# Kernel optimization log

Measured on AMD Instinct MI355X. Metric: run time of the kernel, lower is better.

Reference implementation:

```python
import jax, jax.numpy as jnp
import numpy as np

B, L, IN, H, E = 64, 255, 32, 256, 128
PAD = (L - 1) // 2
DN = ('NCH', 'OIH', 'NCH')


def setup_inputs() -> dict:
    ks = jax.random.split(jax.random.key(0), 10)
    r = lambda k, shp, s=0.05: jax.random.normal(k, shp, dtype=jnp.float32) * s
    return {
        's': jax.random.normal(ks[0], (B, L, IN), dtype=jnp.float32),
        'conv1_w': r(ks[1], (H, IN, L)),
        'conv1_b': r(ks[2], (H,)),
        'bn_gamma': jnp.ones((H,), jnp.float32),
        'bn_beta': jnp.zeros((H,), jnp.float32),
        'conv2_w': r(ks[3], (E, H, L)),
        'conv2_b': r(ks[4], (E,)),
        'pw1': r(ks[5], (E, H, L)),   # stacked Linear(L, H) weights, one per channel
        'pb1': r(ks[6], (E, H)),
        'pw2': r(ks[7], (E, 2, H)),   # stacked Linear(H, 2) weights
        'pb2': r(ks[8], (E, 2)),
    }


def reference(s, conv1_w, conv1_b, bn_gamma, bn_beta, conv2_w, conv2_b, pw1, pb1, pw2, pb2):
    x = jnp.transpose(s, (0, 2, 1))  # (B, IN, T)
    h = jax.lax.conv_general_dilated(x, conv1_w, (1,), [(PAD, PAD)], dimension_numbers=DN)
    h = jax.nn.relu(h + conv1_b[None, :, None])
    # BatchNorm1d in training mode: biased batch stats over (N, T)
    mean = h.mean(axis=(0, 2), keepdims=True)
    var = ((h - mean) ** 2).mean(axis=(0, 2), keepdims=True)
    h = (h - mean) * jax.lax.rsqrt(var + 1e-5) * bn_gamma[None, :, None] + bn_beta[None, :, None]
    z = jax.lax.conv_general_dilated(h, conv2_w, (1,), [(PAD, PAD)], dimension_numbers=DN)
    z = jnp.transpose(z + conv2_b[None, :, None], (0, 2, 1))  # (B, T, E)

    rf = jnp.fft.rfft(z, axis=1)                 # (B, F, E), F = L//2 + 1 == E
    power = jnp.abs(rf)[:, :, 1:] ** 2           # faithful channel-axis slice -> (B, F, E-1)
    freq_bins = jnp.fft.rfftfreq(L)[1:]          # (F-1,) == (E-1,)
    frequency = jnp.sum(freq_bins * power, axis=1) / jnp.sum(power, axis=1)  # (B, E-1)
    amplitude = 2.0 * jnp.sqrt(jnp.sum(power, axis=1)) / L                    # (B, E-1)
    offset = rf.real[:, :, 0] / L                                              # (B, E)

    # batched per-channel 2-layer MLP (replaces Python loop over embedding_dim)
    hmid = jax.nn.relu(jnp.einsum('btc,cht->bch', z, pw1) + pb1[None])  # (B, E, H)
    ang = jnp.einsum('bch,coh->bco', hmid, pw2) + pb2[None]             # (B, E, 2)
    phase = jnp.arctan2(ang[:, :, 1], ang[:, :, 0])                     # (B, E)
    return (amplitude, phase, frequency, offset)
```

## Files before the change

### kernel.cpp

```cpp
#include <hip/hip_runtime.h>
#include <math.h>

#define TB   64
#define TT   255
#define TIN  32
#define NH   256
#define NE   128
#define NK   255
#define NPAD 127

#define NF    384
#define NBINS 193
#define NFC   386
#define FCP   416
#define HCH   64

typedef __attribute__((ext_vector_type(8))) short short8;
typedef __attribute__((ext_vector_type(4))) float float4v;

#define WSB_WP1  0u
#define WSB_Z    0u
#define WSB_HF   8388608u
#define WSB_HMID 8388608u
#define WSB_W2S  25165824u
#define WSB_HSP  37814272u
#define WSB_ZSP  44138496u
#define WSB_BD   56786944u
#define WSB_BW   57182208u
#define WSB_BIT  57577472u
#define WSB_BN   58003456u

#define O_AMP   0u
#define O_PHASE 8128u
#define O_FREQ  16320u
#define O_OFF   24448u

static __device__ __forceinline__ unsigned short f2bf(float f) {
  unsigned int u = __float_as_uint(f);
  unsigned int r = (u + 0x7FFFu + ((u >> 16) & 1u)) >> 16;
  return (unsigned short)r;
}
static __device__ __forceinline__ float bf2f(unsigned short s) {
  return __uint_as_float(((unsigned int)s) << 16);
}
static __device__ __forceinline__ short8 as_s8(uint4 v) {
  union { uint4 u; short8 s; } c; c.u = v; return c.s;
}

static __device__ __forceinline__ void split3(float x, unsigned short& h,
                                              unsigned short& l, unsigned short& m2) {
  h = f2bf(x);
  float r1 = x - bf2f(h);
  l = f2bf(r1);
  m2 = f2bf(r1 - bf2f(l));
}

static __device__ __forceinline__ void stage8(unsigned int* __restrict__ U, int r,
                                              int p0, const float* __restrict__ v) {
  const int sw = r & 7;
  const int base = r * 32;
#pragma unroll
  for (int q = 0; q < 4; ++q) {
    float x0 = v[2 * q], x1 = v[2 * q + 1];
    unsigned short h0 = f2bf(x0), h1 = f2bf(x1);
    unsigned short l0 = f2bf(x0 - bf2f(h0)), l1 = f2bf(x1 - bf2f(h1));
    int p = p0 + q;
    U[base + ((((p >> 2) ^ sw) << 2) | (p & 3))] = (unsigned int)h0 | ((unsigned int)h1 << 16);
    U[base + (((((p >> 2) + 4) ^ sw) << 2) | (p & 3))] = (unsigned int)l0 | ((unsigned int)l1 << 16);
  }
}

static __device__ __forceinline__ void stage8_3(unsigned int* __restrict__ U,
                                                unsigned int* __restrict__ U2, int r,
                                                int p0, const float* __restrict__ v) {
  const int sw = r & 7;
  const int base = r * 32;
#pragma unroll
  for (int q = 0; q < 4; ++q) {
    unsigned short h0, l0, m0_, h1, l1, m1_;
    split3(v[2 * q], h0, l0, m0_);
    split3(v[2 * q + 1], h1, l1, m1_);
    int p = p0 + q;
    int shi = (((p >> 2) ^ sw) << 2) | (p & 3);
    int slo = ((((p >> 2) + 4) ^ sw) << 2) | (p & 3);
    U[base + shi] = (unsigned int)h0 | ((unsigned int)h1 << 16);
    U[base + slo] = (unsigned int)l0 | ((unsigned int)l1 << 16);
    U2[base + shi] = (unsigned int)m0_ | ((unsigned int)m1_ << 16);
  }
}
static __device__ __forceinline__ void stage2_3(unsigned int* __restrict__ U,
                                                unsigned int* __restrict__ U2, int r,
                                                int p, float x0, float x1) {
  const int sw = r & 7;
  unsigned short h0, l0, m0_, h1, l1, m1_;
  split3(x0, h0, l0, m0_);
  split3(x1, h1, l1, m1_);
  int shi = (((p >> 2) ^ sw) << 2) | (p & 3);
  int slo = ((((p >> 2) + 4) ^ sw) << 2) | (p & 3);
  U[r * 32 + shi] = (unsigned int)h0 | ((unsigned int)h1 << 16);
  U[r * 32 + slo] = (unsigned int)l0 | ((unsigned int)l1 << 16);
  U2[r * 32 + shi] = (unsigned int)m0_ | ((unsigned int)m1_ << 16);
}
static __device__ __forceinline__ short8 frag(const unsigned short* __restrict__ lds,
                                              int row, int quad, int part) {
  return *(const short8*)&lds[row * 64 + (((quad ^ (part << 2)) ^ (row & 7)) << 3)];
}
#define MF(a, b, c) __builtin_amdgcn_mfma_f32_16x16x32_bf16((a), (b), (c), 0, 0, 0)
#define MF6(accv, ahv, alv, a2v, bhv, blv, b2v) do {                              \
    accv = MF(ahv, bhv, accv);                                                    \
    accv = MF(ahv, blv, accv);                                                    \
    accv = MF(alv, bhv, accv);                                                    \
    accv = MF(alv, blv, accv);                                                    \
    accv = MF(ahv, b2v, accv);                                                    \
    accv = MF(a2v, bhv, accv);                                                    \
  } while (0)

__global__ __launch_bounds__(256) void bn_zero_k(float* __restrict__ bn) {
  bn[threadIdx.x] = 0.f;
  bn[256 + threadIdx.x] = 0.f;
}

__global__ __launch_bounds__(256) void basis_init_k(float* __restrict__ bd,
                                                    float* __restrict__ bw,
                                                    float* __restrict__ bi_t) {
  const int m = blockIdx.x;
  const int t = threadIdx.x;
  const int f = m >> 1, im = m & 1;
  const float C = 6.28318530717958647692f / 384.f;
  int r1 = (f * t) % 384;
  float th1 = C * (float)r1;
  float s1 = sinf(th1), c1 = cosf(th1);
  float vd = im ? -s1 : c1;
  bd[m * 256 + t] = (t == 255) ? 0.f : vd;
  float wgt = (f == 0 || f == 192) ? 1.f : 2.f;
  bi_t[t * FCP + m] = (im ? -s1 * wgt : c1 * wgt) * (1.f / 384.f);
  if (m < FCP - NFC) bi_t[t * FCP + NFC + m] = 0.f;
  int a = f * (t - 127);
  int r2 = a % 384; if (r2 < 0) r2 += 384;
  float th2 = C * (float)r2;
  float vw = im ? sinf(th2) : cosf(th2);
  bw[m * 256 + t] = (t == 255) ? 0.f : vw;
}

__global__ __launch_bounds__(256) void pack1_k(const float* __restrict__ w1,
                                               unsigned int* __restrict__ wp1u) {
  __shared__ float tile[512][33];
  const int et = blockIdx.x, kc = blockIdx.y;
  const int kk0 = kc * 32, cnt = min(32, NK - kk0);
  const int tid = threadIdx.x;
  for (int idx = tid; idx < 512 * 32; idx += 256) {
    int row = idx >> 5, kl = idx & 31;
    if (kl < cnt) {
      int e_l = row >> 5, i_l = row & 31;
      tile[row][kl] = w1[(size_t)((et * 16 + e_l) * TIN + i_l) * NK + kk0 + kl];
    }
  }
  __syncthreads();
  const int lane = tid >> 2, jp = (tid & 3) * 2;
  const int row0 = (lane & 15) * 32 + (lane >> 4) * 8 + jp;
  for (int kl = 0; kl < cnt; ++kl) {
    float w0 = tile[row0][kl], w1v = tile[row0 + 1][kl];
    unsigned short h0 = f2bf(w0), h1 = f2bf(w1v);
    unsigned short l0 = f2bf(w0 - bf2f(h0)), l1 = f2bf(w1v - bf2f(h1));
    size_t base = (size_t)(kk0 + kl) * 8192 + et * 512 + tid;
    wp1u[base] = (unsigned int)h0 | ((unsigned int)h1 << 16);
    wp1u[base + 256] = (unsigned int)l0 | ((unsigned int)l1 << 16);
  }
}

#define C1_ROWS 384
__global__ __launch_bounds__(256, 2) void conv1_mfma(
    const float* __restrict__ s, const unsigned int* __restrict__ wp1u,
    const float* __restrict__ b1v, float* __restrict__ hf, float* __restrict__ bn) {
  __shared__ __align__(16) unsigned short Alds[C1_ROWS * 64];
  const int th = blockIdx.x & 1, chg = blockIdx.x >> 1, b = blockIdx.y;
  const int tid = threadIdx.x, lane = tid & 63, wv = tid >> 6;
  const int quad = lane >> 4, l15 = lane & 15;
  const int tg = wv & 1, eg = wv >> 1;
  unsigned int* Au = (unsigned int*)Alds;

  for (int idx = tid; idx < C1_ROWS * 16; idx += 256) {
    int r = idx >> 4, p = idx & 15;
    int t = th * 128 + r - NPAD;
    float v0 = 0.f, v1 = 0.f;
    if (t >= 0 && t < TT) {
      const float* sp = &s[(size_t)(b * TT + t) * TIN + p * 2];
      v0 = sp[0]; v1 = sp[1];
    }
    unsigned short h0 = f2bf(v0), h1 = f2bf(v1);
    unsigned short l0 = f2bf(v0 - bf2f(h0)), l1 = f2bf(v1 - bf2f(h1));
    int sw = r & 7;
    Au[r * 32 + ((((p >> 2) ^ sw) << 2) | (p & 3))] = (unsigned int)h0 | ((unsigned int)h1 << 16);
    Au[r * 32 + (((((p >> 2) + 4) ^ sw) << 2) | (p & 3))] = (unsigned int)l0 | ((unsigned int)l1 << 16);
  }

#define LOADB1(buf, KK) do {                                                      \
    const uint4* _b = (const uint4*)(wp1u + (size_t)(KK) * 8192u) +               \
                      (chg * 4 + eg * 2) * 128;                                   \
    buf[0] = _b[lane];          buf[1] = _b[64 + lane];                           \
    buf[2] = _b[128 + lane];    buf[3] = _b[192 + lane];                          \
  } while (0)

#define MSTEP1(KK, buf) do {                                                      \
    short8 bh0 = as_s8(buf[0]), bl0 = as_s8(buf[1]);                              \
    short8 bh1 = as_s8(buf[2]), bl1 = as_s8(buf[3]);                              \
    _Pragma("unroll")                                                             \
    for (int mi = 0; mi < 4; ++mi) {                                              \
      const int row = tg * 64 + mi * 16 + l15 + (KK);                             \
      const int sw = row & 7;                                                     \
      short8 ah = *(const short8*)&Alds[row * 64 + ((quad ^ sw) << 3)];           \
      short8 al = *(const short8*)&Alds[row * 64 + (((quad ^ 4) ^ sw) << 3)];     \
      acc[mi][0] = MF(ah, bh0, acc[mi][0]);                                       \
      acc[mi][0] = MF(ah, bl0, acc[mi][0]);                                       \
      acc[mi][0] = MF(al, bh0, acc[mi][0]);                                       \
      acc[mi][1] = MF(ah, bh1, acc[mi][1]);                                       \
      acc[mi][1] = MF(ah, bl1, acc[mi][1]);                                       \
      acc[mi][1] = MF(al, bh1, acc[mi][1]);                                       \
    }                                                                             \
  } while (0)

  uint4 b0[4], b1x[4], b2x[4];
  LOADB1(b0, 0);
  LOADB1(b1x, 1);
  LOADB1(b2x, 2);
  __syncthreads();

  float4v acc[4][2];
#pragma unroll
  for (int mi = 0; mi < 4; ++mi)
#pragma unroll
    for (int ni = 0; ni < 2; ++ni) acc[mi][ni] = (float4v)(0.f);

  for (int kp = 0; kp < 84; ++kp) {
    const int kk = kp * 3;
    MSTEP1(kk, b0);     LOADB1(b0, kk + 3);
    MSTEP1(kk + 1, b1x); LOADB1(b1x, kk + 4);
    MSTEP1(kk + 2, b2x); LOADB1(b2x, kk + 5);
  }
  MSTEP1(252, b0);
  MSTEP1(253, b1x);
  MSTEP1(254, b2x);

  float s1[2] = {0.f, 0.f}, s2[2] = {0.f, 0.f};
#pragma unroll
  for (int mi = 0; mi < 4; ++mi) {
#pragma unroll
    for (int ni = 0; ni < 2; ++ni) {
      int ch = chg * 64 + (eg * 2 + ni) * 16 + l15;
      float bias = b1v[ch];
#pragma unroll
      for (int r = 0; r < 4; ++r) {
        int t = th * 128 + tg * 64 + mi * 16 + quad * 4 + r;
        if (t < TT) {
          float v = fmaxf(acc[mi][ni][r] + bias, 0.f);
          hf[(size_t)(b * 256 + t) * NH + ch] = v;
          s1[ni] += v; s2[ni] += v * v;
        }
      }
    }
  }
#pragma unroll
  for (int ni = 0; ni < 2; ++ni) {
    s1[ni] += __shfl_xor(s1[ni], 16);
    s1[ni] += __shfl_xor(s1[ni], 32);
    s2[ni] += __shfl_xor(s2[ni], 16);
    s2[ni] += __shfl_xor(s2[ni], 32);
    if (quad == 0) {
      int ch = chg * 64 + (eg * 2 + ni) * 16 + l15;
      atomicAdd(&bn[ch], s1[ni]);
      atomicAdd(&bn[256 + ch], s2[ni]);
    }
  }
#undef LOADB1
#undef MSTEP1
}

__global__ __launch_bounds__(256) void bn_final_k(const float* __restrict__ gamma,
                                                  const float* __restrict__ beta,
                                                  float* __restrict__ bn) {
  const int h = threadIdx.x;
  const float inv = 1.0f / (TB * TT);
  float m = bn[h] * inv;
  float var = bn[256 + h] * inv - m * m;
  float sc = gamma[h] / sqrtf(var + 1e-5f);
  bn[512 + h] = sc;
  bn[768 + h] = beta[h] - m * sc;
}


__global__ __launch_bounds__(256, 2) void w2prep_mfma(
    const float* __restrict__ w2, const float* __restrict__ bw,
    float* __restrict__ W, int h0c) {
  __shared__ __align__(16) unsigned short Alds[128 * 64];
  __shared__ __align__(16) unsigned short A2lds[128 * 64];
  __shared__ __align__(16) unsigned short Blds[128 * 64];
  __shared__ __align__(16) unsigned short B2lds[128 * 64];
  const int n0 = blockIdx.x * 128, m0 = blockIdx.y * 128;
  const int tid = threadIdx.x, lane = tid & 63, wv = tid >> 6;
  const int quad = lane >> 4, l15 = lane & 15;
  const int wm = wv >> 1, wn = wv & 1;
  unsigned int* Au = (unsigned int*)Alds;
  unsigned int* A2u = (unsigned int*)A2lds;
  unsigned int* Bu = (unsigned int*)Blds;
  unsigned int* B2u = (unsigned int*)B2lds;

  float4v acc[4][4];
#pragma unroll
  for (int i = 0; i < 4; ++i)
#pragma unroll
    for (int j = 0; j < 4; ++j) acc[i][j] = (float4v)(0.f);

  const int rA = tid >> 1, hfA = tid & 1;
  const int fcA = m0 + rA;
  const float* srcA = bw + fcA * 256;
  const int rB = tid >> 1, hfB = tid & 1;
  const int eB = (n0 + rB) >> 6, hlB = (n0 + rB) & 63;
  const float* srcB = w2 + ((size_t)(eB * NH + h0c + hlB)) * NK;

  for (int kk = 0; kk < 8; ++kk) {
    const int k0 = kk * 32;
    if (kk) __syncthreads();
    {
      float va[16];
      if (fcA < NFC) {
        const float4* s4 = (const float4*)(srcA + k0 + hfA * 16);
        *(float4*)(va + 0) = s4[0]; *(float4*)(va + 4) = s4[1];
        *(float4*)(va + 8) = s4[2]; *(float4*)(va + 12) = s4[3];
      } else {
#pragma unroll
        for (int q = 0; q < 16; ++q) va[q] = 0.f;
      }
      stage8_3(Au, A2u, rA, hfA * 8, va);
      stage8_3(Au, A2u, rA, hfA * 8 + 4, va + 8);
    }
    {
      float vb[16];
#pragma unroll
      for (int q = 0; q < 16; ++q) {
        int k = k0 + hfB * 16 + q;
        vb[q] = (k < NK) ? srcB[k] : 0.f;
      }
      stage8_3(Bu, B2u, rB, hfB * 8, vb);
      stage8_3(Bu, B2u, rB, hfB * 8 + 4, vb + 8);
    }
    __syncthreads();
    short8 bh[4], bl[4], b2[4];
#pragma unroll
    for (int ni = 0; ni < 4; ++ni) {
      int rb = wn * 64 + ni * 16 + l15;
      bh[ni] = frag(Blds, rb, quad, 0);
      bl[ni] = frag(Blds, rb, quad, 1);
      b2[ni] = frag(B2lds, rb, quad, 0);
    }
#pragma unroll
    for (int mi = 0; mi < 4; ++mi) {
      int ra = wm * 64 + mi * 16 + l15;
      short8 ah = frag(Alds, ra, quad, 0);
      short8 al = frag(Alds, ra, quad, 1);
      short8 a2 = frag(A2lds, ra, quad, 0);
#pragma unroll
      for (int ni = 0; ni < 4; ++ni) MF6(acc[mi][ni], ah, al, a2, bh[ni], bl[ni], b2[ni]);
    }
  }
#pragma unroll
  for (int mi = 0; mi < 4; ++mi) {
    int fc0 = m0 + wm * 64 + mi * 16 + quad * 4;
#pragma unroll
    for (int ni = 0; ni < 4; ++ni) {
      int n = n0 + wn * 64 + ni * 16 + l15;
#pragma unroll
      for (int r = 0; r < 4; ++r) {
        if (fc0 + r < NFC) W[(size_t)(fc0 + r) * 8192 + n] = acc[mi][ni][r];
      }
    }
  }
}

__global__ __launch_bounds__(256, 2) void dftH_mfma(
    const float* __restrict__ hf, const float* __restrict__ bn,
    const float* __restrict__ bd, float* __restrict__ H, int h0c) {
  __shared__ __align__(16) unsigned short Alds[128 * 64];
  __shared__ __align__(16) unsigned short A2lds[128 * 64];
  __shared__ __align__(16) unsigned short Blds[128 * 64];
  __shared__ __align__(16) unsigned short B2lds[128 * 64];
  const int n0 = blockIdx.x * 128, m0 = blockIdx.y * 128;
  const int b0 = n0 >> 6;
  const int tid = threadIdx.x, lane = tid & 63, wv = tid >> 6;
  const int quad = lane >> 4, l15 = lane & 15;
  const int wm = wv >> 1, wn = wv & 1;
  const int g = tid >> 6;
  unsigned int* Au = (unsigned int*)Alds;
  unsigned int* A2u = (unsigned int*)A2lds;
  unsigned int* Bu = (unsigned int*)Blds;
  unsigned int* B2u = (unsigned int*)B2lds;
  const float scL = bn[512 + h0c + lane];
  const float shL = bn[768 + h0c + lane];

  float4v acc[4][4];
#pragma unroll
  for (int i = 0; i < 4; ++i)
#pragma unroll
    for (int j = 0; j < 4; ++j) acc[i][j] = (float4v)(0.f);

  const int rA = tid >> 1, hfA = tid & 1;
  const int fcA = m0 + rA;
  const float* srcA = bd + fcA * 256;

  for (int kk = 0; kk < 8; ++kk) {
    const int k0 = kk * 32;
    if (kk) __syncthreads();
    {
      float va[16];
      if (fcA < NFC) {
        const float4* s4 = (const float4*)(srcA + k0 + hfA * 16);
        *(float4*)(va + 0) = s4[0]; *(float4*)(va + 4) = s4[1];
        *(float4*)(va + 8) = s4[2]; *(float4*)(va + 12) = s4[3];
      } else {
#pragma unroll
        for (int q = 0; q < 16; ++q) va[q] = 0.f;
      }
      stage8_3(Au, A2u, rA, hfA * 8, va);
      stage8_3(Au, A2u, rA, hfA * 8 + 4, va + 8);
    }
#pragma unroll
    for (int i = 0; i < 8; ++i) {
      int combo = i * 4 + g;
      int tp = combo >> 1, bl_ = combo & 1;
      int t0 = k0 + tp * 2;
      int b = b0 + bl_;
      float v0 = (t0 < TT)
          ? fmaf(hf[(size_t)(b * 256 + t0) * NH + h0c + lane], scL, shL) : 0.f;
      float v1 = (t0 + 1 < TT)
          ? fmaf(hf[(size_t)(b * 256 + t0 + 1) * NH + h0c + lane], scL, shL) : 0.f;
      stage2_3(Bu, B2u, bl_ * 64 + lane, tp, v0, v1);
    }
    __syncthreads();
    short8 bh[4], bl[4], b2[4];
#pragma unroll
    for (int ni = 0; ni < 4; ++ni) {
      int rb = wn * 64 + ni * 16 + l15;
      bh[ni] = frag(Blds, rb, quad, 0);
      bl[ni] = frag(Blds, rb, quad, 1);
      b2[ni] = frag(B2lds, rb, quad, 0);
    }
#pragma unroll
    for (int mi = 0; mi < 4; ++mi) {
      int ra = wm * 64 + mi * 16 + l15;
      short8 ah = frag(Alds, ra, quad, 0);
      short8 al = frag(Alds, ra, quad, 1);
      short8 a2 = frag(A2lds, ra, quad, 0);
#pragma unroll
      for (int ni = 0; ni < 4; ++ni) MF6(acc[mi][ni], ah, al, a2, bh[ni], bl[ni], b2[ni]);
    }
  }
#pragma unroll
  for (int mi = 0; mi < 4; ++mi) {
    int fc0 = m0 + wm * 64 + mi * 16 + quad * 4;
#pragma unroll
    for (int ni = 0; ni < 4; ++ni) {
      int n = n0 + wn * 64 + ni * 16 + l15;
#pragma unroll
      for (int r = 0; r < 4; ++r) {
        if (fc0 + r < NFC) H[(size_t)(fc0 + r) * 4096 + n] = acc[mi][ni][r];
      }
    }
  }
}

__global__ __launch_bounds__(256, 2) void fgemm_mfma(
    const float* __restrict__ H, const float* __restrict__ W,
    float* __restrict__ zsp, int first) {
  __shared__ __align__(16) unsigned short Alds[64 * 64];
  __shared__ __align__(16) unsigned short A2lds[64 * 64];
  __shared__ __align__(16) unsigned short Blds[128 * 64];
  __shared__ __align__(16) unsigned short B2lds[128 * 64];
  const int ri = blockIdx.x, f = blockIdx.y;
  const int tid = threadIdx.x, lane = tid & 63, wv = tid >> 6;
  const int quad = lane >> 4, l15 = lane & 15;
  const int wm = wv >> 1, wn = wv & 1;
  unsigned int* Au = (unsigned int*)Alds;
  unsigned int* A2u = (unsigned int*)A2lds;
  unsigned int* Bu = (unsigned int*)Blds;
  unsigned int* B2u = (unsigned int*)B2lds;

  float4v acc[2][4];
#pragma unroll
  for (int i = 0; i < 2; ++i)
#pragma unroll
    for (int j = 0; j < 4; ++j) acc[i][j] = (float4v)(0.f);

  const int rA = tid >> 2, qA = tid & 3;
  const int rB = tid >> 1, hB = tid & 1;

  for (int kk = 0; kk < 4; ++kk) {
    const int ca = kk >> 1;
    const int hb = (kk & 1) * 32;
    if (kk) __syncthreads();
    {
      float va[8];
      const float4* s4 = (const float4*)(H + (size_t)(2 * f + ca) * 4096 + rA * 64 + hb + qA * 8);
      *(float4*)(va + 0) = s4[0]; *(float4*)(va + 4) = s4[1];
      stage8_3(Au, A2u, rA, qA * 4, va);
    }
    {
      const int cb = ri ^ (kk >> 1);
      const int neg = (ri == 0 && kk >= 2);
      float vb[16];
      const float4* s4 = (const float4*)(W + (size_t)(2 * f + cb) * 8192 + rB * 64 + hb + hB * 16);
      *(float4*)(vb + 0) = s4[0]; *(float4*)(vb + 4) = s4[1];
      *(float4*)(vb + 8) = s4[2]; *(float4*)(vb + 12) = s4[3];
      if (neg) {
#pragma unroll
        for (int q = 0; q < 16; ++q) vb[q] = -vb[q];
      }
      stage8_3(Bu, B2u, rB, hB * 8, vb);
      stage8_3(Bu, B2u, rB, hB * 8 + 4, vb + 8);
    }
    __syncthreads();
    short8 bh[4], bl[4], b2[4];
#pragma unroll
    for (int ni = 0; ni < 4; ++ni) {
      int rb = wn * 64 + ni * 16 + l15;
      bh[ni] = frag(Blds, rb, quad, 0);
      bl[ni] = frag(Blds, rb, quad, 1);
      b2[ni] = frag(B2lds, rb, quad, 0);
    }
#pragma unroll
    for (int mi = 0; mi < 2; ++mi) {
      int ra = wm * 32 + mi * 16 + l15;
      short8 ah = frag(Alds, ra, quad, 0);
      short8 al = frag(Alds, ra, quad, 1);
      short8 a2 = frag(A2lds, ra, quad, 0);
#pragma unroll
      for (int ni = 0; ni < 4; ++ni) MF6(acc[mi][ni], ah, al, a2, bh[ni], bl[ni], b2[ni]);
    }
  }
  float* Z = zsp + (size_t)(2 * f + ri) * 8192;
#pragma unroll
  for (int mi = 0; mi < 2; ++mi) {
#pragma unroll
    for (int ni = 0; ni < 4; ++ni) {
      int e = wn * 64 + ni * 16 + l15;
#pragma unroll
      for (int r = 0; r < 4; ++r) {
        int b = wm * 32 + mi * 16 + quad * 4 + r;
        size_t off = (size_t)b * 128 + e;
        if (first) Z[off] = acc[mi][ni][r];
        else       Z[off] += acc[mi][ni][r];
      }
    }
  }
}

__global__ __launch_bounds__(256, 2) void idft_mfma(
    const float* __restrict__ zsp, const float* __restrict__ bi_t,
    const float* __restrict__ b2, float* __restrict__ z) {
  __shared__ __align__(16) unsigned short Alds[128 * 64];
  __shared__ __align__(16) unsigned short A2lds[128 * 64];
  __shared__ __align__(16) unsigned short Blds[128 * 64];
  __shared__ __align__(16) unsigned short B2lds[128 * 64];
  const int n0 = blockIdx.x * 128, m0 = blockIdx.y * 128;
  const int tid = threadIdx.x, lane = tid & 63, wv = tid >> 6;
  const int quad = lane >> 4, l15 = lane & 15;
  const int wm = wv >> 1, wn = wv & 1;
  const int g = tid >> 6;
  unsigned int* Au = (unsigned int*)Alds;
  unsigned int* A2u = (unsigned int*)A2lds;
  unsigned int* Bu = (unsigned int*)Blds;
  unsigned int* B2u = (unsigned int*)B2lds;

  float4v acc[4][4];
#pragma unroll
  for (int i = 0; i < 4; ++i)
#pragma unroll
    for (int j = 0; j < 4; ++j) acc[i][j] = (float4v)(0.f);

  const int rB = tid >> 1, hB = tid & 1;

  for (int kk = 0; kk < 13; ++kk) {
    const int k0 = kk * 32;
    if (kk) __syncthreads();
#pragma unroll
    for (int i = 0; i < 8; ++i) {
      int combo = i * 4 + g;
      int tp = combo >> 1, beh = combo & 1;
      int fc0 = k0 + tp * 2;
      int row = beh * 64 + lane;
      float v0 = (fc0 < NFC) ? zsp[(size_t)fc0 * 8192 + m0 + row] : 0.f;
      float v1 = (fc0 + 1 < NFC) ? zsp[(size_t)(fc0 + 1) * 8192 + m0 + row] : 0.f;
      stage2_3(Au, A2u, row, tp, v0, v1);
    }
    {
      float vb[16];
      const float4* s4 = (const float4*)(bi_t + (size_t)(n0 + rB) * FCP + k0 + hB * 16);
      *(float4*)(vb + 0) = s4[0]; *(float4*)(vb + 4) = s4[1];
      *(float4*)(vb + 8) = s4[2]; *(float4*)(vb + 12) = s4[3];
      stage8_3(Bu, B2u, rB, hB * 8, vb);
      stage8_3(Bu, B2u, rB, hB * 8 + 4, vb + 8);
    }
    __syncthreads();
    short8 bh[4], bl[4], b2[4];
#pragma unroll
    for (int ni = 0; ni < 4; ++ni) {
      int rb = wn * 64 + ni * 16 + l15;
      bh[ni] = frag(Blds, rb, quad, 0);
      bl[ni] = frag(Blds, rb, quad, 1);
      b2[ni] = frag(B2lds, rb, quad, 0);
    }
#pragma unroll
    for (int mi = 0; mi < 4; ++mi) {
      int ra = wm * 64 + mi * 16 + l15;
      short8 ah = frag(Alds, ra, quad, 0);
      short8 al = frag(Alds, ra, quad, 1);
      short8 a2 = frag(A2lds, ra, quad, 0);
#pragma unroll
      for (int ni = 0; ni < 4; ++ni) MF6(acc[mi][ni], ah, al, a2, bh[ni], bl[ni], b2[ni]);
    }
  }
#pragma unroll
  for (int mi = 0; mi < 4; ++mi) {
#pragma unroll
    for (int ni = 0; ni < 4; ++ni) {
      int t = n0 + wn * 64 + ni * 16 + l15;
#pragma unroll
      for (int r = 0; r < 4; ++r) {
        int be = m0 + wm * 64 + mi * 16 + quad * 4 + r;
        if (t < TT) z[(size_t)be * TT + t] = acc[mi][ni][r] + b2[be & 127];
      }
    }
  }
}

__global__ __launch_bounds__(256) void mlp1_k(const float* __restrict__ z,
                                              const float* __restrict__ pw1,
                                              const float* __restrict__ pb1,
                                              float* __restrict__ hmid) {
  const int TC = 128;
  __shared__ float zl[TC * 68];
  __shared__ float pl[TC * 68];
  const int c = blockIdx.y, h0 = blockIdx.x * 64, tid = threadIdx.x;
  const int h4 = tid & 15, b4 = tid >> 4;
  float acc[4][4];
#pragma unroll
  for (int a = 0; a < 4; ++a)
#pragma unroll
    for (int bb = 0; bb < 4; ++bb) acc[a][bb] = 0.f;
  for (int t0 = 0; t0 < TT; t0 += TC) {
    const int tc = min(TC, TT - t0);
    __syncthreads();
    for (int idx = tid; idx < 64 * tc; idx += 256) {
      int r = idx / tc, t = idx - r * tc;
      zl[t * 68 + r] = z[(size_t)(r * NE + c) * TT + t0 + t];
      pl[t * 68 + r] = pw1[(size_t)(c * NH + h0 + r) * TT + t0 + t];
    }
    __syncthreads();
    for (int t = 0; t < tc; ++t) {
      float4 zv = *(const float4*)&zl[t * 68 + b4 * 4];
      float4 pv = *(const float4*)&pl[t * 68 + h4 * 4];
      float zz[4] = {zv.x, zv.y, zv.z, zv.w};
      float pp[4] = {pv.x, pv.y, pv.z, pv.w};
#pragma unroll
      for (int a = 0; a < 4; ++a)
#pragma unroll
        for (int bb = 0; bb < 4; ++bb) acc[a][bb] = fmaf(pp[a], zz[bb], acc[a][bb]);
    }
  }
#pragma unroll
  for (int a = 0; a < 4; ++a) {
    int hh = h0 + h4 * 4 + a;
    float bias = pb1[c * NH + hh];
#pragma unroll
    for (int bb = 0; bb < 4; ++bb) {
      int bidx = b4 * 4 + bb;
      float v = acc[a][bb] + bias;
      hmid[(size_t)(bidx * NE + c) * NH + hh] = fmaxf(v, 0.f);
    }
  }
}

__global__ __launch_bounds__(256) void mlp2_k(const float* __restrict__ hmid,
                                              const float* __restrict__ pw2,
                                              const float* __restrict__ pb2,
                                              float* __restrict__ out) {
  const int tid = threadIdx.x, lane = tid & 63, wv = tid >> 6;
  const int p = blockIdx.x * 4 + wv;
  const int b = p >> 7, c = p & 127;
  const float4 hv = *(const float4*)&hmid[(size_t)(b * NE + c) * NH + lane * 4];
  const float4 p0 = *(const float4*)&pw2[(size_t)(c * 2 + 0) * NH + lane * 4];
  const float4 p1 = *(const float4*)&pw2[(size_t)(c * 2 + 1) * NH + lane * 4];
  float s0 = hv.x * p0.x + hv.y * p0.y + hv.z * p0.z + hv.w * p0.w;
  float s1 = hv.x * p1.x + hv.y * p1.y + hv.z * p1.z + hv.w * p1.w;
#pragma unroll
  for (int off = 32; off; off >>= 1) {
    s0 += __shfl_down(s0, off);
    s1 += __shfl_down(s1, off);
  }
  if (lane == 0) {
    float a0 = s0 + pb2[c * 2 + 0];
    float a1 = s1 + pb2[c * 2 + 1];
    out[O_PHASE + b * NE + c] = atan2f(a1, a0);
  }
}

__global__ __launch_bounds__(256) void amp_k(const float* __restrict__ z,
                                             float* __restrict__ out) {
  const int tid = threadIdx.x, lane = tid & 63, wv = tid >> 6;
  const int b = blockIdx.x, c = blockIdx.y * 4 + wv;
  const float* row = z + (size_t)(b * NE + c) * TT;
  float s1 = 0.f, s2 = 0.f;
  for (int idx = lane; idx < TT; idx += 64) {
    float v = row[idx];
    s1 += v; s2 += v * v;
  }
#pragma unroll
  for (int off = 32; off; off >>= 1) {
    s1 += __shfl_down(s1, off);
    s2 += __shfl_down(s2, off);
  }
  if (lane == 0 && c >= 1) {
    float P = 0.5f * (255.f * s2 + s1 * s1);
    out[O_AMP + b * 127 + (c - 1)] = 2.f * sqrtf(P) / 255.f;
    out[O_FREQ + b * 127 + (c - 1)] = (float)c / 255.f;
  }
}

__global__ __launch_bounds__(128) void offset_k(const float* __restrict__ z,
                                                float* __restrict__ out) {
  __shared__ float zr[TT];
  __shared__ float ct[TT];
  const int b = blockIdx.x, tid = threadIdx.x;
  for (int idx = tid; idx < TT; idx += 128) {
    zr[idx] = z[(size_t)(b * NE + 0) * TT + idx];
    ct[idx] = cosf(6.283185307179586f * (float)idx / 255.f);
  }
  __syncthreads();
  const int f = tid;
  float s = 0.f;
  int m = 0;
  for (int t = 0; t < TT; ++t) {
    s += zr[t] * ct[m];
    m += f; if (m >= TT) m -= TT;
  }
  out[O_OFF + b * NE + f] = s / 255.f;
}

extern "C" void kernel_launch(void* const* d_in, const int* in_sizes, int n_in,
                              void* d_out, int out_size, void* d_ws, size_t ws_size,
                              hipStream_t stream) {
  (void)in_sizes; (void)n_in; (void)out_size; (void)ws_size;
  const float* s       = (const float*)d_in[0];
  const float* conv1_w = (const float*)d_in[1];
  const float* conv1_b = (const float*)d_in[2];
  const float* bn_g    = (const float*)d_in[3];
  const float* bn_b    = (const float*)d_in[4];
  const float* conv2_w = (const float*)d_in[5];
  const float* conv2_b = (const float*)d_in[6];
  const float* pw1     = (const float*)d_in[7];
  const float* pb1     = (const float*)d_in[8];
  const float* pw2     = (const float*)d_in[9];
  const float* pb2     = (const float*)d_in[10];
  float* out = (float*)d_out;
  char* ws   = (char*)d_ws;

  unsigned int* wp1u = (unsigned int*)(ws + WSB_WP1);
  float* z    = (float*)(ws + WSB_Z);
  float* hf   = (float*)(ws + WSB_HF);
  float* hmid = (float*)(ws + WSB_HMID);
  float* W2s  = (float*)(ws + WSB_W2S);
  float* Hs   = (float*)(ws + WSB_HSP);
  float* zsp  = (float*)(ws + WSB_ZSP);
  float* bd   = (float*)(ws + WSB_BD);
  float* bwt  = (float*)(ws + WSB_BW);
  float* bit  = (float*)(ws + WSB_BIT);
  float* bn   = (float*)(ws + WSB_BN);

  bn_zero_k<<<1, 256, 0, stream>>>(bn);
  basis_init_k<<<NFC, 256, 0, stream>>>(bd, bwt, bit);
  pack1_k<<<dim3(16, 8), 256, 0, stream>>>(conv1_w, wp1u);

  conv1_mfma<<<dim3(8, TB), 256, 0, stream>>>(s, wp1u, conv1_b, hf, bn);
  bn_final_k<<<1, 256, 0, stream>>>(bn_g, bn_b, bn);

  for (int c = 0; c < 4; ++c) {
    w2prep_mfma<<<dim3(64, 4), 256, 0, stream>>>(conv2_w, bwt, W2s, c * HCH);
    dftH_mfma<<<dim3(32, 4), 256, 0, stream>>>(hf, bn, bd, Hs, c * HCH);
    fgemm_mfma<<<dim3(2, NBINS), 256, 0, stream>>>(Hs, W2s, zsp, c == 0 ? 1 : 0);
  }
  idft_mfma<<<dim3(2, 64), 256, 0, stream>>>(zsp, bit, conv2_b, z);

  mlp1_k<<<dim3(4, NE), 256, 0, stream>>>(z, pw1, pb1, hmid);
  mlp2_k<<<TB * NE / 4, 256, 0, stream>>>(hmid, pw2, pb2, out);
  amp_k<<<dim3(TB, 32), 256, 0, stream>>>(z, out);
  offset_k<<<TB, 128, 0, stream>>>(z, out);
}
```

Measured before the change: 725.8 us.

## Pre-split DFT bases into bf16 planes and fold batchnorm affine into DFT output

Basis matrices for the DFT, w2 transform and inverse DFT are now written once as packed hi/lo/mid bf16 planes, so GEMM kernels load them directly instead of re-splitting floats on every tile. conv1 stores its activations as packed hi+lo bf16, and the batchnorm scale/shift is applied after the DFT using a precomputed basis row-sum d1. This lets dftH run 5 MFMAs per fragment instead of 6 and drop one LDS buffer. The w2prep B loads are reorganised for coalescing, and the dftH and idft tiles are halved on N to launch more blocks. Storing hf as two bf16 parts gives slightly less precision than fp32.

```diff
diff --git a/kernel.cpp b/kernel.cpp
--- a/kernel.cpp
+++ b/kernel.cpp
@@ -20,15 +20,22 @@
 
 #define WSB_WP1  0u
 #define WSB_Z    0u
-#define WSB_HF   8388608u
+#define WSB_HFU  8388608u
 #define WSB_HMID 8388608u
 #define WSB_W2S  25165824u
 #define WSB_HSP  37814272u
+#define WSB_BIH  37814272u
+#define WSB_BIL  38027264u
+#define WSB_BIM  38240256u
 #define WSB_ZSP  44138496u
-#define WSB_BD   56786944u
-#define WSB_BW   57182208u
-#define WSB_BIT  57577472u
-#define WSB_BN   58003456u
+#define WSB_BDH  56786944u
+#define WSB_BDL  56984576u
+#define WSB_BDM  57182208u
+#define WSB_BWH  57379840u
+#define WSB_BWL  57577472u
+#define WSB_BWM  57775104u
+#define WSB_D1   57972736u
+#define WSB_BN   57974528u
 
 #define O_AMP   0u
 #define O_PHASE 8128u
@@ -54,52 +61,46 @@
   l = f2bf(r1);
   m2 = f2bf(r1 - bf2f(l));
 }
-
-static __device__ __forceinline__ void stage8(unsigned int* __restrict__ U, int r,
-                                              int p0, const float* __restrict__ v) {
+static __device__ __forceinline__ void split_pack2(float x0, float x1,
+    unsigned int& ph, unsigned int& pl, unsigned int& pm) {
+  unsigned short h0, l0, m0_, h1, l1, m1_;
+  split3(x0, h0, l0, m0_);
+  split3(x1, h1, l1, m1_);
+  ph = (unsigned int)h0 | ((unsigned int)h1 << 16);
+  pl = (unsigned int)l0 | ((unsigned int)l1 << 16);
+  pm = (unsigned int)m0_ | ((unsigned int)m1_ << 16);
+}
+
+static __device__ __forceinline__ void put_hi(unsigned int* __restrict__ U, int r,
+                                              int p, unsigned int v) {
   const int sw = r & 7;
-  const int base = r * 32;
-#pragma unroll
-  for (int q = 0; q < 4; ++q) {
-    float x0 = v[2 * q], x1 = v[2 * q + 1];
-    unsigned short h0 = f2bf(x0), h1 = f2bf(x1);
-    unsigned short l0 = f2bf(x0 - bf2f(h0)), l1 = f2bf(x1 - bf2f(h1));
-    int p = p0 + q;
-    U[base + ((((p >> 2) ^ sw) << 2) | (p & 3))] = (unsigned int)h0 | ((unsigned int)h1 << 16);
-    U[base + (((((p >> 2) + 4) ^ sw) << 2) | (p & 3))] = (unsigned int)l0 | ((unsigned int)l1 << 16);
-  }
-}
-
+  U[r * 32 + ((((p >> 2) ^ sw) << 2) | (p & 3))] = v;
+}
+static __device__ __forceinline__ void put_lo(unsigned int* __restrict__ U, int r,
+                                              int p, unsigned int v) {
+  const int sw = r & 7;
+  U[r * 32 + (((((p >> 2) + 4) ^ sw) << 2) | (p & 3))] = v;
+}
 static __device__ __forceinline__ void stage8_3(unsigned int* __restrict__ U,
                                                 unsigned int* __restrict__ U2, int r,
                                                 int p0, const float* __restrict__ v) {
-  const int sw = r & 7;
-  const int base = r * 32;
 #pragma unroll
   for (int q = 0; q < 4; ++q) {
-    unsigned short h0, l0, m0_, h1, l1, m1_;
-    split3(v[2 * q], h0, l0, m0_);
-    split3(v[2 * q + 1], h1, l1, m1_);
-    int p = p0 + q;
-    int shi = (((p >> 2) ^ sw) << 2) | (p & 3);
-    int slo = ((((p >> 2) + 4) ^ sw) << 2) | (p & 3);
-    U[base + shi] = (unsigned int)h0 | ((unsigned int)h1 << 16);
-    U[base + slo] = (unsigned int)l0 | ((unsigned int)l1 << 16);
-    U2[base + shi] = (unsigned int)m0_ | ((unsigned int)m1_ << 16);
+    unsigned int ph, pl, pm;
+    split_pack2(v[2 * q], v[2 * q + 1], ph, pl, pm);
+    put_hi(U, r, p0 + q, ph);
+    put_lo(U, r, p0 + q, pl);
+    put_hi(U2, r, p0 + q, pm);
   }
 }
 static __device__ __forceinline__ void stage2_3(unsigned int* __restrict__ U,
                                                 unsigned int* __restrict__ U2, int r,
                                                 int p, float x0, float x1) {
-  const int sw = r & 7;
-  unsigned short h0, l0, m0_, h1, l1, m1_;
-  split3(x0, h0, l0, m0_);
-  split3(x1, h1, l1, m1_);
-  int shi = (((p >> 2) ^ sw) << 2) | (p & 3);
-  int slo = ((((p >> 2) + 4) ^ sw) << 2) | (p & 3);
-  U[r * 32 + shi] = (unsigned int)h0 | ((unsigned int)h1 << 16);
-  U[r * 32 + slo] = (unsigned int)l0 | ((unsigned int)l1 << 16);
-  U2[r * 32 + shi] = (unsigned int)m0_ | ((unsigned int)m1_ << 16);
+  unsigned int ph, pl, pm;
+  split_pack2(x0, x1, ph, pl, pm);
+  put_hi(U, r, p, ph);
+  put_lo(U, r, p, pl);
+  put_hi(U2, r, p, pm);
 }
 static __device__ __forceinline__ short8 frag(const unsigned short* __restrict__ lds,
                                               int row, int quad, int part) {
@@ -114,32 +115,78 @@
     accv = MF(ahv, b2v, accv);                                                    \
     accv = MF(a2v, bhv, accv);                                                    \
   } while (0)
+#define MF5(accv, ahv, alv, a2v, bhv, blv) do {                                   \
+    accv = MF(ahv, bhv, accv);                                                    \
+    accv = MF(ahv, blv, accv);                                                    \
+    accv = MF(alv, bhv, accv);                                                    \
+    accv = MF(alv, blv, accv);                                                    \
+    accv = MF(a2v, bhv, accv);                                                    \
+  } while (0)
 
 __global__ __launch_bounds__(256) void bn_zero_k(float* __restrict__ bn) {
   bn[threadIdx.x] = 0.f;
   bn[256 + threadIdx.x] = 0.f;
 }
 
-__global__ __launch_bounds__(256) void basis_init_k(float* __restrict__ bd,
-                                                    float* __restrict__ bw,
-                                                    float* __restrict__ bi_t) {
+__global__ __launch_bounds__(256) void basis_init_k(
+    unsigned int* __restrict__ bdh, unsigned int* __restrict__ bdl,
+    unsigned int* __restrict__ bdm, unsigned int* __restrict__ bwh,
+    unsigned int* __restrict__ bwl, unsigned int* __restrict__ bwm) {
+  __shared__ float sv[2][256];
   const int m = blockIdx.x;
   const int t = threadIdx.x;
   const int f = m >> 1, im = m & 1;
   const float C = 6.28318530717958647692f / 384.f;
   int r1 = (f * t) % 384;
   float th1 = C * (float)r1;
-  float s1 = sinf(th1), c1 = cosf(th1);
-  float vd = im ? -s1 : c1;
-  bd[m * 256 + t] = (t == 255) ? 0.f : vd;
-  float wgt = (f == 0 || f == 192) ? 1.f : 2.f;
-  bi_t[t * FCP + m] = (im ? -s1 * wgt : c1 * wgt) * (1.f / 384.f);
-  if (m < FCP - NFC) bi_t[t * FCP + NFC + m] = 0.f;
+  sv[0][t] = (t == 255) ? 0.f : (im ? -sinf(th1) : cosf(th1));
   int a = f * (t - 127);
   int r2 = a % 384; if (r2 < 0) r2 += 384;
   float th2 = C * (float)r2;
-  float vw = im ? sinf(th2) : cosf(th2);
-  bw[m * 256 + t] = (t == 255) ? 0.f : vw;
+  sv[1][t] = (t == 255) ? 0.f : (im ? sinf(th2) : cosf(th2));
+  __syncthreads();
+  const int which = t >> 7, j = t & 127;
+  unsigned int ph, pl, pm;
+  split_pack2(sv[which][2 * j], sv[which][2 * j + 1], ph, pl, pm);
+  size_t off = (size_t)m * 128 + j;
+  if (which == 0) { bdh[off] = ph; bdl[off] = pl; bdm[off] = pm; }
+  else            { bwh[off] = ph; bwl[off] = pl; bwm[off] = pm; }
+}
+
+__global__ __launch_bounds__(256) void d1_k(float* __restrict__ d1) {
+  const int fc = blockIdx.x * 256 + threadIdx.x;
+  if (fc >= NFC) return;
+  const int f = fc >> 1, im = fc & 1;
+  const float C = 6.28318530717958647692f / 384.f;
+  float s = 0.f;
+  int r = 0;
+  for (int t = 0; t < TT; ++t) {
+    float th = C * (float)r;
+    s += im ? -sinf(th) : cosf(th);
+    r += f; if (r >= 384) r -= 384;
+  }
+  d1[fc] = s;
+}
+
+__global__ __launch_bounds__(256) void basis_bi_k(
+    unsigned int* __restrict__ bih, unsigned int* __restrict__ bil,
+    unsigned int* __restrict__ bim) {
+  const int kp = blockIdx.x;
+  const int t = threadIdx.x;
+  float x0 = 0.f, x1 = 0.f;
+  if (kp < NBINS) {
+    const int f = kp;
+    const float C = 6.28318530717958647692f / 384.f;
+    int r1 = (f * t) % 384;
+    float th = C * (float)r1;
+    float wgt = ((f == 0 || f == 192) ? 1.f : 2.f) * (1.f / 384.f);
+    x0 = cosf(th) * wgt;
+    x1 = -sinf(th) * wgt;
+  }
+  unsigned int ph, pl, pm;
+  split_pack2(x0, x1, ph, pl, pm);
+  size_t off = (size_t)kp * 256 + t;
+  bih[off] = ph; bil[off] = pl; bim[off] = pm;
 }
 
 __global__ __launch_bounds__(256) void pack1_k(const float* __restrict__ w1,
@@ -171,7 +218,8 @@
 #define C1_ROWS 384
 __global__ __launch_bounds__(256, 2) void conv1_mfma(
     const float* __restrict__ s, const unsigned int* __restrict__ wp1u,
-    const float* __restrict__ b1v, float* __restrict__ hf, float* __restrict__ bn) {
+    const float* __restrict__ b1v, unsigned int* __restrict__ hfu,
+    float* __restrict__ bn) {
   __shared__ __align__(16) unsigned short Alds[C1_ROWS * 64];
   const int th = blockIdx.x & 1, chg = blockIdx.x >> 1, b = blockIdx.y;
   const int tid = threadIdx.x, lane = tid & 63, wv = tid >> 6;
@@ -253,7 +301,10 @@
         int t = th * 128 + tg * 64 + mi * 16 + quad * 4 + r;
         if (t < TT) {
           float v = fmaxf(acc[mi][ni][r] + bias, 0.f);
-          hf[(size_t)(b * 256 + t) * NH + ch] = v;
+          unsigned short vh = f2bf(v);
+          unsigned short vl = f2bf(v - bf2f(vh));
+          hfu[(size_t)(b * 256 + t) * NH + ch] =
+              (unsigned int)vh | ((unsigned int)vl << 16);
           s1[ni] += v; s2[ni] += v * v;
         }
       }
@@ -288,8 +339,34 @@
 }
 
 
+#define LOAD_A_PLANES(PH, PL, PM) do {                                            \
+    if (fcA < NFC) {                                                              \
+      size_t ab = (size_t)fcA * 128 + (k0 >> 1) + hfA * 8;                        \
+      uint4 h0v = *(const uint4*)(PH + ab), h1v = *(const uint4*)(PH + ab + 4);   \
+      uint4 l0v = *(const uint4*)(PL + ab), l1v = *(const uint4*)(PL + ab + 4);   \
+      uint4 m0v = *(const uint4*)(PM + ab), m1v = *(const uint4*)(PM + ab + 4);   \
+      _Pragma("unroll")                                                           \
+      for (int q = 0; q < 4; ++q) {                                               \
+        put_hi(Au, rA, hfA * 8 + q, ((const unsigned int*)&h0v)[q]);              \
+        put_hi(Au, rA, hfA * 8 + 4 + q, ((const unsigned int*)&h1v)[q]);          \
+        put_lo(Au, rA, hfA * 8 + q, ((const unsigned int*)&l0v)[q]);              \
+        put_lo(Au, rA, hfA * 8 + 4 + q, ((const unsigned int*)&l1v)[q]);          \
+        put_hi(A2u, rA, hfA * 8 + q, ((const unsigned int*)&m0v)[q]);             \
+        put_hi(A2u, rA, hfA * 8 + 4 + q, ((const unsigned int*)&m1v)[q]);         \
+      }                                                                           \
+    } else {                                                                      \
+      _Pragma("unroll")                                                           \
+      for (int q = 0; q < 8; ++q) {                                               \
+        put_hi(Au, rA, hfA * 8 + q, 0u);                                          \
+        put_lo(Au, rA, hfA * 8 + q, 0u);                                          \
+        put_hi(A2u, rA, hfA * 8 + q, 0u);                                         \
+      }                                                                           \
+    }                                                                             \
+  } while (0)
+
 __global__ __launch_bounds__(256, 2) void w2prep_mfma(
-    const float* __restrict__ w2, const float* __restrict__ bw,
+    const float* __restrict__ w2, const unsigned int* __restrict__ bwh,
+    const unsigned int* __restrict__ bwl, const unsigned int* __restrict__ bwm,
     float* __restrict__ W, int h0c) {
   __shared__ __align__(16) unsigned short Alds[128 * 64];
   __shared__ __align__(16) unsigned short A2lds[128 * 64];
@@ -312,36 +389,24 @@
 
   const int rA = tid >> 1, hfA = tid & 1;
   const int fcA = m0 + rA;
-  const float* srcA = bw + fcA * 256;
-  const int rB = tid >> 1, hfB = tid & 1;
-  const int eB = (n0 + rB) >> 6, hlB = (n0 + rB) & 63;
-  const float* srcB = w2 + ((size_t)(eB * NH + h0c + hlB)) * NK;
+  const int lane8 = tid & 7, rsub = tid >> 3;
 
   for (int kk = 0; kk < 8; ++kk) {
     const int k0 = kk * 32;
     if (kk) __syncthreads();
-    {
-      float va[16];
-      if (fcA < NFC) {
-        const float4* s4 = (const float4*)(srcA + k0 + hfA * 16);
-        *(float4*)(va + 0) = s4[0]; *(float4*)(va + 4) = s4[1];
-        *(float4*)(va + 8) = s4[2]; *(float4*)(va + 12) = s4[3];
-      } else {
-#pragma unroll
-        for (int q = 0; q < 16; ++q) va[q] = 0.f;
-      }
-      stage8_3(Au, A2u, rA, hfA * 8, va);
-      stage8_3(Au, A2u, rA, hfA * 8 + 4, va + 8);
-    }
-    {
-      float vb[16];
-#pragma unroll
-      for (int q = 0; q < 16; ++q) {
-        int k = k0 + hfB * 16 + q;
-        vb[q] = (k < NK) ? srcB[k] : 0.f;
-      }
-      stage8_3(Bu, B2u, rB, hfB * 8, vb);
-      stage8_3(Bu, B2u, rB, hfB * 8 + 4, vb + 8);
+    LOAD_A_PLANES(bwh, bwl, bwm);
+#pragma unroll
+    for (int pass = 0; pass < 4; ++pass) {
+      int row = pass * 32 + rsub;
+      int e = (n0 + row) >> 6, hl = (n0 + row) & 63;
+      const float* src = w2 + ((size_t)(e * NH + h0c + hl)) * NK;
+      int kb = k0 + lane8 * 4;
+      float f0 = (kb < NK) ? src[kb] : 0.f;
+      float f1 = (kb + 1 < NK) ? src[kb + 1] : 0.f;
+      float f2 = (kb + 2 < NK) ? src[kb + 2] : 0.f;
+      float f3 = (kb + 3 < NK) ? src[kb + 3] : 0.f;
+      stage2_3(Bu, B2u, row, lane8 * 2, f0, f1);
+      stage2_3(Bu, B2u, row, lane8 * 2 + 1, f2, f3);
     }
     __syncthreads();
     short8 bh[4], bl[4], b2[4];
@@ -377,71 +442,55 @@
 }
 
 __global__ __launch_bounds__(256, 2) void dftH_mfma(
-    const float* __restrict__ hf, const float* __restrict__ bn,
-    const float* __restrict__ bd, float* __restrict__ H, int h0c) {
+    const unsigned int* __restrict__ hfu, const float* __restrict__ bn,
+    const unsigned int* __restrict__ bdh, const unsigned int* __restrict__ bdl,
+    const unsigned int* __restrict__ bdm, const float* __restrict__ d1,
+    float* __restrict__ H, int h0c) {
   __shared__ __align__(16) unsigned short Alds[128 * 64];
   __shared__ __align__(16) unsigned short A2lds[128 * 64];
-  __shared__ __align__(16) unsigned short Blds[128 * 64];
-  __shared__ __align__(16) unsigned short B2lds[128 * 64];
-  const int n0 = blockIdx.x * 128, m0 = blockIdx.y * 128;
-  const int b0 = n0 >> 6;
+  __shared__ __align__(16) unsigned short Blds[64 * 64];
+  const int b = blockIdx.x, m0 = blockIdx.y * 128;
   const int tid = threadIdx.x, lane = tid & 63, wv = tid >> 6;
   const int quad = lane >> 4, l15 = lane & 15;
   const int wm = wv >> 1, wn = wv & 1;
-  const int g = tid >> 6;
+  const int hl = tid & 63, g = tid >> 6;
   unsigned int* Au = (unsigned int*)Alds;
   unsigned int* A2u = (unsigned int*)A2lds;
   unsigned int* Bu = (unsigned int*)Blds;
-  unsigned int* B2u = (unsigned int*)B2lds;
-  const float scL = bn[512 + h0c + lane];
-  const float shL = bn[768 + h0c + lane];
-
-  float4v acc[4][4];
+
+  float4v acc[4][2];
 #pragma unroll
   for (int i = 0; i < 4; ++i)
 #pragma unroll
-    for (int j = 0; j < 4; ++j) acc[i][j] = (float4v)(0.f);
+    for (int j = 0; j < 2; ++j) acc[i][j] = (float4v)(0.f);
 
   const int rA = tid >> 1, hfA = tid & 1;
   const int fcA = m0 + rA;
-  const float* srcA = bd + fcA * 256;
 
   for (int kk = 0; kk < 8; ++kk) {
     const int k0 = kk * 32;
     if (kk) __syncthreads();
-    {
-      float va[16];
-      if (fcA < NFC) {
-        const float4* s4 = (const float4*)(srcA + k0 + hfA * 16);
-        *(float4*)(va + 0) = s4[0]; *(float4*)(va + 4) = s4[1];
-        *(float4*)(va + 8) = s4[2]; *(float4*)(va + 12) = s4[3];
-      } else {
-#pragma unroll
-        for (int q = 0; q < 16; ++q) va[q] = 0.f;
-      }
-      stage8_3(Au, A2u, rA, hfA * 8, va);
-      stage8_3(Au, A2u, rA, hfA * 8 + 4, va + 8);
-    }
-#pragma unroll
-    for (int i = 0; i < 8; ++i) {
-      int combo = i * 4 + g;
-      int tp = combo >> 1, bl_ = combo & 1;
+    LOAD_A_PLANES(bdh, bdl, bdm);
+#pragma unroll
+    for (int j = 0; j < 4; ++j) {
+      int tp = g * 4 + j;
       int t0 = k0 + tp * 2;
-      int b = b0 + bl_;
-      float v0 = (t0 < TT)
-          ? fmaf(hf[(size_t)(b * 256 + t0) * NH + h0c + lane], scL, shL) : 0.f;
-      float v1 = (t0 + 1 < TT)
-          ? fmaf(hf[(size_t)(b * 256 + t0 + 1) * NH + h0c + lane], scL, shL) : 0.f;
-      stage2_3(Bu, B2u, bl_ * 64 + lane, tp, v0, v1);
+      unsigned int u0 = (t0 < TT)
+          ? hfu[(size_t)(b * 256 + t0) * NH + h0c + hl] : 0u;
+      unsigned int u1 = (t0 + 1 < TT)
+          ? hfu[(size_t)(b * 256 + t0 + 1) * NH + h0c + hl] : 0u;
+      unsigned int hp = (u0 & 0xFFFFu) | ((u1 & 0xFFFFu) << 16);
+      unsigned int lp = (u0 >> 16) | (u1 & 0xFFFF0000u);
+      put_hi(Bu, hl, tp, hp);
+      put_lo(Bu, hl, tp, lp);
     }
     __syncthreads();
-    short8 bh[4], bl[4], b2[4];
-#pragma unroll
-    for (int ni = 0; ni < 4; ++ni) {
-      int rb = wn * 64 + ni * 16 + l15;
+    short8 bh[2], bl[2];
+#pragma unroll
+    for (int ni = 0; ni < 2; ++ni) {
+      int rb = wn * 32 + ni * 16 + l15;
       bh[ni] = frag(Blds, rb, quad, 0);
       bl[ni] = frag(Blds, rb, quad, 1);
-      b2[ni] = frag(B2lds, rb, quad, 0);
     }
 #pragma unroll
     for (int mi = 0; mi < 4; ++mi) {
@@ -450,18 +499,22 @@
       short8 al = frag(Alds, ra, quad, 1);
       short8 a2 = frag(A2lds, ra, quad, 0);
 #pragma unroll
-      for (int ni = 0; ni < 4; ++ni) MF6(acc[mi][ni], ah, al, a2, bh[ni], bl[ni], b2[ni]);
+      for (int ni = 0; ni < 2; ++ni) MF5(acc[mi][ni], ah, al, a2, bh[ni], bl[ni]);
     }
   }
 #pragma unroll
   for (int mi = 0; mi < 4; ++mi) {
     int fc0 = m0 + wm * 64 + mi * 16 + quad * 4;
 #pragma unroll
-    for (int ni = 0; ni < 4; ++ni) {
-      int n = n0 + wn * 64 + ni * 16 + l15;
+    for (int ni = 0; ni < 2; ++ni) {
+      int hli = wn * 32 + ni * 16 + l15;
+      float scv = bn[512 + h0c + hli];
+      float shv = bn[768 + h0c + hli];
 #pragma unroll
       for (int r = 0; r < 4; ++r) {
-        if (fc0 + r < NFC) H[(size_t)(fc0 + r) * 4096 + n] = acc[mi][ni][r];
+        int fc = fc0 + r;
+        if (fc < NFC)
+          H[(size_t)fc * 4096 + b * 64 + hli] = scv * acc[mi][ni][r] + shv * d1[fc];
       }
     }
   }
@@ -553,29 +606,28 @@
 }
 
 __global__ __launch_bounds__(256, 2) void idft_mfma(
-    const float* __restrict__ zsp, const float* __restrict__ bi_t,
+    const float* __restrict__ zsp, const unsigned int* __restrict__ bih,
+    const unsigned int* __restrict__ bil, const unsigned int* __restrict__ bim,
     const float* __restrict__ b2, float* __restrict__ z) {
   __shared__ __align__(16) unsigned short Alds[128 * 64];
   __shared__ __align__(16) unsigned short A2lds[128 * 64];
-  __shared__ __align__(16) unsigned short Blds[128 * 64];
-  __shared__ __align__(16) unsigned short B2lds[128 * 64];
-  const int n0 = blockIdx.x * 128, m0 = blockIdx.y * 128;
+  __shared__ __align__(16) unsigned short Blds[64 * 64];
+  __shared__ __align__(16) unsigned short B2lds[64 * 64];
+  const int n0 = blockIdx.x * 64, m0 = blockIdx.y * 128;
   const int tid = threadIdx.x, lane = tid & 63, wv = tid >> 6;
   const int quad = lane >> 4, l15 = lane & 15;
   const int wm = wv >> 1, wn = wv & 1;
-  const int g = tid >> 6;
+  const int tl = tid & 63, g = tid >> 6;
   unsigned int* Au = (unsigned int*)Alds;
   unsigned int* A2u = (unsigned int*)A2lds;
   unsigned int* Bu = (unsigned int*)Blds;
   unsigned int* B2u = (unsigned int*)B2lds;
 
-  float4v acc[4][4];
+  float4v acc[4][2];
 #pragma unroll
   for (int i = 0; i < 4; ++i)
 #pragma unroll
-    for (int j = 0; j < 4; ++j) acc[i][j] = (float4v)(0.f);
-
-  const int rB = tid >> 1, hB = tid & 1;
+    for (int j = 0; j < 2; ++j) acc[i][j] = (float4v)(0.f);
 
   for (int kk = 0; kk < 13; ++kk) {
     const int k0 = kk * 32;
@@ -590,22 +642,22 @@
       float v1 = (fc0 + 1 < NFC) ? zsp[(size_t)(fc0 + 1) * 8192 + m0 + row] : 0.f;
       stage2_3(Au, A2u, row, tp, v0, v1);
     }
-    {
-      float vb[16];
-      const float4* s4 = (const float4*)(bi_t + (size_t)(n0 + rB) * FCP + k0 + hB * 16);
-      *(float4*)(vb + 0) = s4[0]; *(float4*)(vb + 4) = s4[1];
-      *(float4*)(vb + 8) = s4[2]; *(float4*)(vb + 12) = s4[3];
-      stage8_3(Bu, B2u, rB, hB * 8, vb);
-      stage8_3(Bu, B2u, rB, hB * 8 + 4, vb + 8);
+#pragma unroll
+    for (int j = 0; j < 4; ++j) {
+      int tp = g * 4 + j;
+      size_t off = (size_t)((k0 >> 1) + tp) * 256 + n0 + tl;
+      put_hi(Bu, tl, tp, bih[off]);
+      put_lo(Bu, tl, tp, bil[off]);
+      put_hi(B2u, tl, tp, bim[off]);
     }
     __syncthreads();
-    short8 bh[4], bl[4], b2[4];
-#pragma unroll
-    for (int ni = 0; ni < 4; ++ni) {
-      int rb = wn * 64 + ni * 16 + l15;
+    short8 bh[2], bl[2], b2f[2];
+#pragma unroll
+    for (int ni = 0; ni < 2; ++ni) {
+      int rb = wn * 32 + ni * 16 + l15;
       bh[ni] = frag(Blds, rb, quad, 0);
       bl[ni] = frag(Blds, rb, quad, 1);
-      b2[ni] = frag(B2lds, rb, quad, 0);
+      b2f[ni] = frag(B2lds, rb, quad, 0);
     }
 #pragma unroll
     for (int mi = 0; mi < 4; ++mi) {
@@ -614,14 +666,14 @@
       short8 al = frag(Alds, ra, quad, 1);
       short8 a2 = frag(A2lds, ra, quad, 0);
 #pragma unroll
-      for (int ni = 0; ni < 4; ++ni) MF6(acc[mi][ni], ah, al, a2, bh[ni], bl[ni], b2[ni]);
+      for (int ni = 0; ni < 2; ++ni) MF6(acc[mi][ni], ah, al, a2, bh[ni], bl[ni], b2f[ni]);
     }
   }
 #pragma unroll
   for (int mi = 0; mi < 4; ++mi) {
 #pragma unroll
-    for (int ni = 0; ni < 4; ++ni) {
-      int t = n0 + wn * 64 + ni * 16 + l15;
+    for (int ni = 0; ni < 2; ++ni) {
+      int t = n0 + wn * 32 + ni * 16 + l15;
 #pragma unroll
       for (int r = 0; r < 4; ++r) {
         int be = m0 + wm * 64 + mi * 16 + quad * 4 + r;
@@ -764,29 +816,38 @@
 
   unsigned int* wp1u = (unsigned int*)(ws + WSB_WP1);
   float* z    = (float*)(ws + WSB_Z);
-  float* hf   = (float*)(ws + WSB_HF);
+  unsigned int* hfu = (unsigned int*)(ws + WSB_HFU);
   float* hmid = (float*)(ws + WSB_HMID);
   float* W2s  = (float*)(ws + WSB_W2S);
   float* Hs   = (float*)(ws + WSB_HSP);
   float* zsp  = (float*)(ws + WSB_ZSP);
-  float* bd   = (float*)(ws + WSB_BD);
-  float* bwt  = (float*)(ws + WSB_BW);
-  float* bit  = (float*)(ws + WSB_BIT);
-  float* bn   = (float*)(ws + WSB_BN);
+  unsigned int* bdh = (unsigned int*)(ws + WSB_BDH);
+  unsigned int* bdl = (unsigned int*)(ws + WSB_BDL);
+  unsigned int* bdm = (unsigned int*)(ws + WSB_BDM);
+  unsigned int* bwh = (unsigned int*)(ws + WSB_BWH);
+  unsigned int* bwl = (unsigned int*)(ws + WSB_BWL);
+  unsigned int* bwm = (unsigned int*)(ws + WSB_BWM);
+  unsigned int* bih = (unsigned int*)(ws + WSB_BIH);
+  unsigned int* bil = (unsigned int*)(ws + WSB_BIL);
+  unsigned int* bim = (unsigned int*)(ws + WSB_BIM);
+  float* d1 = (float*)(ws + WSB_D1);
+  float* bn = (float*)(ws + WSB_BN);
 
   bn_zero_k<<<1, 256, 0, stream>>>(bn);
-  basis_init_k<<<NFC, 256, 0, stream>>>(bd, bwt, bit);
+  basis_init_k<<<NFC, 256, 0, stream>>>(bdh, bdl, bdm, bwh, bwl, bwm);
+  d1_k<<<2, 256, 0, stream>>>(d1);
   pack1_k<<<dim3(16, 8), 256, 0, stream>>>(conv1_w, wp1u);
 
-  conv1_mfma<<<dim3(8, TB), 256, 0, stream>>>(s, wp1u, conv1_b, hf, bn);
+  conv1_mfma<<<dim3(8, TB), 256, 0, stream>>>(s, wp1u, conv1_b, hfu, bn);
   bn_final_k<<<1, 256, 0, stream>>>(bn_g, bn_b, bn);
 
   for (int c = 0; c < 4; ++c) {
-    w2prep_mfma<<<dim3(64, 4), 256, 0, stream>>>(conv2_w, bwt, W2s, c * HCH);
-    dftH_mfma<<<dim3(32, 4), 256, 0, stream>>>(hf, bn, bd, Hs, c * HCH);
+    w2prep_mfma<<<dim3(64, 4), 256, 0, stream>>>(conv2_w, bwh, bwl, bwm, W2s, c * HCH);
+    dftH_mfma<<<dim3(64, 4), 256, 0, stream>>>(hfu, bn, bdh, bdl, bdm, d1, Hs, c * HCH);
     fgemm_mfma<<<dim3(2, NBINS), 256, 0, stream>>>(Hs, W2s, zsp, c == 0 ? 1 : 0);
   }
-  idft_mfma<<<dim3(2, 64), 256, 0, stream>>>(zsp, bit, conv2_b, z);
+  basis_bi_k<<<208, 256, 0, stream>>>(bih, bil, bim);
+  idft_mfma<<<dim3(4, 64), 256, 0, stream>>>(zsp, bih, bil, bim, conv2_b, z);
 
   mlp1_k<<<dim3(4, NE), 256, 0, stream>>>(z, pw1, pb1, hmid);
   mlp2_k<<<TB * NE / 4, 256, 0, stream>>>(hmid, pw2, pb2, out);
```

New measurement: 729.4 us. Within noise of the previous version (+0.5%).
